# Performance work log

Hardware: AMD Instinct MI355X
Metric: run time of the kernel (lower is better)

The kernel has to match this reference:

```python
import jax, jax.numpy as jnp
import numpy as np

N, E, F_IN, H, C = 50000, 800000, 256, 64, 40
NEG_SLOPE = 0.2


def setup_inputs() -> dict:
    key = jax.random.key(0)
    ks = jax.random.split(key, 16)
    sc = lambda fan: 1.0 / np.sqrt(fan)
    return {
        "x": jax.random.normal(ks[0], (N, F_IN), dtype=jnp.float32),
        "edge_index": jax.random.randint(ks[1], (2, E), 0, N, dtype=jnp.int64),
        "W1l": jax.random.normal(ks[2], (F_IN, H), dtype=jnp.float32) * sc(F_IN),
        "b1l": jnp.zeros((H,), jnp.float32),
        "W1r": jax.random.normal(ks[3], (F_IN, H), dtype=jnp.float32) * sc(F_IN),
        "b1r": jnp.zeros((H,), jnp.float32),
        "att1": jax.random.normal(ks[4], (H,), dtype=jnp.float32) * sc(H),
        "bias1": jnp.zeros((H,), jnp.float32),
        "lin1_W": jax.random.normal(ks[5], (F_IN, H), dtype=jnp.float32) * sc(F_IN),
        "lin1_b": jnp.zeros((H,), jnp.float32),
        "W2l": jax.random.normal(ks[6], (H, C), dtype=jnp.float32) * sc(H),
        "b2l": jnp.zeros((C,), jnp.float32),
        "W2r": jax.random.normal(ks[7], (H, C), dtype=jnp.float32) * sc(H),
        "b2r": jnp.zeros((C,), jnp.float32),
        "att2": jax.random.normal(ks[8], (C,), dtype=jnp.float32) * sc(C),
        "bias2": jnp.zeros((C,), jnp.float32),
        "lin2_W": jax.random.normal(ks[9], (H, C), dtype=jnp.float32) * sc(H),
        "lin2_b": jnp.zeros((C,), jnp.float32),
    }


def gatv2_layer(x, src, dst, Wl, bl, Wr, br, att, bias, n):
    # PyG GATv2Conv, heads=1: xl = lin_l(x) (source), xr = lin_r(x) (target)
    xl = x @ Wl + bl                               # [n, out]
    xr = x @ Wr + br                               # [n, out]
    m = xl[src] + xr[dst]                          # [E, out] per-edge gather
    e = jax.nn.leaky_relu(m, NEG_SLOPE) @ att      # [E] attention logits
    # segment softmax over destination nodes (self-loops guarantee nonempty segments)
    emax = jax.ops.segment_max(e, dst, num_segments=n)
    ee = jnp.exp(e - emax[dst])
    denom = jax.ops.segment_sum(ee, dst, num_segments=n)
    alpha = ee / denom[dst]                        # [E]
    out = jax.ops.segment_sum(alpha[:, None] * xl[src], dst, num_segments=n)
    return out + bias


def reference(x, edge_index, W1l, b1l, W1r, b1r, att1, bias1, lin1_W, lin1_b,
              W2l, b2l, W2r, b2r, att2, bias2, lin2_W, lin2_b):
    n = x.shape[0]
    loops = jnp.arange(n, dtype=edge_index.dtype)
    src = jnp.concatenate([edge_index[0], loops])  # add_self_loops=True (PyG default)
    dst = jnp.concatenate([edge_index[1], loops])
    h = jax.nn.relu(gatv2_layer(x, src, dst, W1l, b1l, W1r, b1r, att1, bias1, n)
                    + x @ lin1_W + lin1_b)
    o = (gatv2_layer(h, src, dst, W2l, b2l, W2r, b2r, att2, bias2, n)
         + h @ lin2_W + lin2_b)
    return jax.nn.log_softmax(o, axis=1), edge_index
```

## Files before the change

kernel.cpp:

```cpp
#include <hip/hip_runtime.h>
#include <cmath>

#define NN 50000
#define NP 50048
#define NE 800000
#define CD 40
#define NEG_SLOPE 0.2f
#define NITEMS (NE + NN)
#define CHUNK 2048
#define NCH 416
#define NBKT 391
#define BCAP 3072
#define GB1 782
#define TB1 (3 * 64 * 256)
#define TB2 (3 * 64 * 64)
#define WPB 240

typedef __attribute__((ext_vector_type(8))) short s16x8;
typedef __attribute__((ext_vector_type(4))) float f32x4;
typedef __attribute__((ext_vector_type(2))) float f32x2;

__device__ __forceinline__ f32x2 pk_fma(f32x2 a, f32x2 b, f32x2 c) {
#if __has_builtin(__builtin_elementwise_fma)
  return __builtin_elementwise_fma(a, b, c);
#else
  f32x2 r; r[0] = fmaf(a[0], b[0], c[0]); r[1] = fmaf(a[1], b[1], c[1]); return r;
#endif
}
__device__ __forceinline__ f32x2 pk_max(f32x2 a, f32x2 b) {
#if __has_builtin(__builtin_elementwise_max)
  return __builtin_elementwise_max(a, b);
#else
  f32x2 r; r[0] = fmaxf(a[0], b[0]); r[1] = fmaxf(a[1], b[1]); return r;
#endif
}

__device__ __forceinline__ short f2bf(float x) {
  unsigned u = __builtin_bit_cast(unsigned, x);
  u += 0x7fffu + ((u >> 16) & 1u);
  return (short)(u >> 16);
}
__device__ __forceinline__ unsigned pack2(float lo, float hi) {
  return (unsigned)(unsigned short)f2bf(lo) | ((unsigned)(unsigned short)f2bf(hi) << 16);
}
__device__ __forceinline__ float bf2f_lo(unsigned v) {
  return __builtin_bit_cast(float, v << 16);
}
__device__ __forceinline__ float bf2f_hi(unsigned v) {
  return __builtin_bit_cast(float, v & 0xffff0000u);
}
__device__ __forceinline__ void ldbf8v(const unsigned short* p, f32x2* f) {
  const uint4 v = *reinterpret_cast<const uint4*>(p);
  f[0] = (f32x2){bf2f_lo(v.x), bf2f_hi(v.x)};
  f[1] = (f32x2){bf2f_lo(v.y), bf2f_hi(v.y)};
  f[2] = (f32x2){bf2f_lo(v.z), bf2f_hi(v.z)};
  f[3] = (f32x2){bf2f_lo(v.w), bf2f_hi(v.w)};
}

__global__ __launch_bounds__(256) void prep_bin(const float* __restrict__ W1l,
                                                const float* __restrict__ W1r,
                                                const float* __restrict__ L1,
                                                const float* __restrict__ W2l,
                                                const float* __restrict__ W2r,
                                                const float* __restrict__ L2,
                                                short* __restrict__ Wp1,
                                                short* __restrict__ Wp2,
                                                const int* __restrict__ ei,
                                                float* __restrict__ outE,
                                                int* __restrict__ gcur,
                                                unsigned* __restrict__ rec) {
  const int tid = threadIdx.x;
  if (blockIdx.x < WPB) {
    int e = blockIdx.x * 256 + tid;
    if (e < TB1) {
      int kb = e / 6144, r = e % 6144;
      int w = r / 2048, r2 = r % 2048;
      int t = r2 / 512, r3 = r2 % 512;
      int lane = r3 / 8, j = r3 % 8;
      int n = t * 16 + (lane & 15);
      int k = kb * 32 + (lane >> 4) * 8 + j;
      const float* W = (w == 0) ? W1l : (w == 1) ? W1r : L1;
      Wp1[e] = f2bf(W[k * 64 + n]);
    } else {
      e -= TB1;
      int kb = e / 6144, r = e % 6144;
      int w = r / 2048, r2 = r % 2048;
      int t = r2 / 512, r3 = r2 % 512;
      int lane = r3 / 8, j = r3 % 8;
      int n = t * 16 + (lane & 15);
      int k = kb * 32 + (lane >> 4) * 8 + j;
      const float* W = (w == 0) ? W2l : (w == 1) ? W2r : L2;
      Wp2[e] = (n < 40) ? f2bf(W[k * 40 + n]) : (short)0;
    }
    return;
  }
  __shared__ unsigned sorted[CHUNK];
  __shared__ int hist[512];
  __shared__ int bcur[512];
  __shared__ int gbase[512];
  const int base = (blockIdx.x - WPB) * CHUNK;
  for (int t = tid; t < 512; t += 256) { hist[t] = 0; bcur[t] = 0; gbase[t] = 0; }
  __syncthreads();
  unsigned key[CHUNK / 256];
#pragma unroll
  for (int u = 0; u < CHUNK / 256; ++u) {
    const int j = base + u * 256 + tid;
    unsigned k = 0xFFFFFFFFu;
    if (j < NITEMS) {
      int s, d;
      if (j < NE) {
        s = ei[j]; d = ei[NE + j];
        outE[j] = (float)s; outE[NE + j] = (float)d;
      } else {
        s = j - NE; d = s;
      }
      k = ((unsigned)d << 16) | (unsigned)s;
      atomicAdd(&hist[k >> 23], 1);
    }
    key[u] = k;
  }
  __syncthreads();
  if (tid < 64) {
    int carry = 0;
#pragma unroll
    for (int c = 0; c < 8; ++c) {
      int v = hist[c * 64 + tid];
      int inc = v;
#pragma unroll
      for (int off = 1; off < 64; off <<= 1) {
        int tt = __shfl_up(inc, off, 64);
        if (tid >= off) inc += tt;
      }
      hist[c * 64 + tid] = carry + inc - v;
      carry += __shfl(inc, 63, 64);
    }
  }
  __syncthreads();
#pragma unroll
  for (int u = 0; u < CHUNK / 256; ++u) {
    const unsigned k = key[u];
    if (k != 0xFFFFFFFFu) {
      const int b = k >> 23;
      sorted[hist[b] + atomicAdd(&bcur[b], 1)] = k;
    }
  }
  __syncthreads();
  for (int t = tid; t < NBKT; t += 256) {
    const int c = bcur[t];
    if (c > 0) gbase[t] = atomicAdd(&gcur[t], c);
  }
  __syncthreads();
  const int cnt = min(CHUNK, NITEMS - base);
  for (int i = tid; i < cnt; i += 256) {
    const unsigned k = sorted[i];
    const int b = k >> 23;
    const int p = gbase[b] + (i - hist[b]);
    if (p < BCAP) rec[(size_t)b * BCAP + p] = k;
  }
}

__device__ __forceinline__ void gemm1_body(int bid, const float* __restrict__ X,
                                           const short* __restrict__ Wp,
                                           const float* __restrict__ B0,
                                           const float* __restrict__ B1,
                                           const float* __restrict__ B2,
                                           unsigned short* __restrict__ Y0,
                                           unsigned short* __restrict__ Y1,
                                           unsigned short* __restrict__ Y2) {
  const int lane = threadIdx.x & 63;
  const int wave = threadIdx.x >> 6;
  const int r0 = bid * 64 + wave * 16;
  const int m = lane & 15;
  const int q = lane >> 4;
  f32x4 acc[3][4] = {};
  const float* a0 = X + (size_t)min(r0 + m, NN - 1) * 256 + q * 8;
  const short* bp = Wp + lane * 8;
#pragma unroll
  for (int kb = 0; kb < 8; ++kb) {
    const float4 v0 = *reinterpret_cast<const float4*>(a0 + kb * 32);
    const float4 v1 = *reinterpret_cast<const float4*>(a0 + kb * 32 + 4);
    s16x8 af0;
    af0[0] = f2bf(v0.x); af0[1] = f2bf(v0.y); af0[2] = f2bf(v0.z); af0[3] = f2bf(v0.w);
    af0[4] = f2bf(v1.x); af0[5] = f2bf(v1.y); af0[6] = f2bf(v1.z); af0[7] = f2bf(v1.w);
#pragma unroll
    for (int w = 0; w < 3; ++w) {
#pragma unroll
      for (int t = 0; t < 4; ++t) {
        const s16x8 bf = *reinterpret_cast<const s16x8*>(
            bp + (size_t)((kb * 3 + w) * 4 + t) * 512);
        acc[w][t] = __builtin_amdgcn_mfma_f32_16x16x32_bf16(af0, bf, acc[w][t], 0, 0, 0);
      }
    }
  }
#pragma unroll
  for (int w = 0; w < 3; ++w) {
    const float* B = (w == 0) ? B0 : (w == 1) ? B1 : B2;
    unsigned short* Y = (w == 0) ? Y0 : (w == 1) ? Y1 : Y2;
#pragma unroll
    for (int t = 0; t < 4; ++t) {
      const int c = t * 16 + m;
      const float bv = B[c];
#pragma unroll
      for (int rg = 0; rg < 4; ++rg) {
        const int row = r0 + q * 4 + rg;
        if (row < NN)
          Y[(size_t)row * 64 + c] = (unsigned short)f2bf(acc[w][t][rg] + bv);
      }
    }
  }
}

__global__ __launch_bounds__(256, 2) void build_gemm1(
    const float* __restrict__ X, const short* __restrict__ Wp1,
    const float* __restrict__ B0, const float* __restrict__ B1,
    const float* __restrict__ B2, unsigned short* __restrict__ Y0,
    unsigned short* __restrict__ Y1, unsigned short* __restrict__ Y2,
    const int* __restrict__ gcur, const unsigned* __restrict__ rec,
    int* __restrict__ offsets, unsigned short* __restrict__ csr16) {
  if (blockIdx.x < GB1) {
    gemm1_body(blockIdx.x, X, Wp1, B0, B1, B2, Y0, Y1, Y2);
    return;
  }
  const int b = blockIdx.x - GB1;
  const int tid = threadIdx.x;
  __shared__ unsigned recs[BCAP];
  __shared__ int red[256];
  __shared__ int cnt[128];
  __shared__ int sc[128];
  __shared__ int cur[128];
  int acc = 0;
  for (int t = tid; t < NBKT; t += 256)
    if (t < b) acc += gcur[t];
  red[tid] = acc;
  __syncthreads();
#pragma unroll
  for (int off = 128; off >= 1; off >>= 1) {
    if (tid < off) red[tid] += red[tid + off];
    __syncthreads();
  }
  const int base = red[0];
  const int Tb = min(gcur[b], BCAP);
  if (tid < 128) cnt[tid] = 0;
  __syncthreads();
  for (int i = tid; i < Tb; i += 256) {
    const unsigned k = rec[(size_t)b * BCAP + i];
    recs[i] = k;
    atomicAdd(&cnt[(k >> 16) & 127], 1);
  }
  __syncthreads();
  if (tid < 128) sc[tid] = cnt[tid];
  __syncthreads();
#pragma unroll
  for (int off = 1; off < 128; off <<= 1) {
    int v = (tid < 128 && tid >= off) ? sc[tid - off] : 0;
    __syncthreads();
    if (tid < 128) sc[tid] += v;
    __syncthreads();
  }
  if (tid < 128) {
    const int n = b * 128 + tid;
    if (n < NN) offsets[n + 1] = base + sc[tid];
    cur[tid] = sc[tid] - cnt[tid];
  }
  if (b == 0 && tid == 0) offsets[0] = 0;
  __syncthreads();
  for (int i = tid; i < Tb; i += 256) {
    const unsigned k = recs[i];
    const int p = atomicAdd(&cur[(k >> 16) & 127], 1);
    csr16[base + p] = (unsigned short)(k & 0xFFFFu);
  }
}

__global__ __launch_bounds__(256) void gemm2(const short* __restrict__ Xb,
                                             const short* __restrict__ Wp,
                                             const float* __restrict__ B0,
                                             const float* __restrict__ B1,
                                             const float* __restrict__ B2,
                                             unsigned short* __restrict__ Y0,
                                             unsigned short* __restrict__ Y1,
                                             unsigned short* __restrict__ Y2) {
  const int lane = threadIdx.x & 63;
  const int wave = threadIdx.x >> 6;
  const int r0 = blockIdx.x * 64 + wave * 16;
  const int m = lane & 15;
  const int q = lane >> 4;
  f32x4 acc[3][4] = {};
  const short* a0 = Xb + (size_t)(r0 + m) * 64 + q * 8;
  const short* bp = Wp + lane * 8;
#pragma unroll
  for (int kb = 0; kb < 2; ++kb) {
    const s16x8 af0 = *reinterpret_cast<const s16x8*>(a0 + kb * 32);
#pragma unroll
    for (int w = 0; w < 3; ++w) {
#pragma unroll
      for (int t = 0; t < 4; ++t) {
        const s16x8 bf = *reinterpret_cast<const s16x8*>(
            bp + (size_t)((kb * 3 + w) * 4 + t) * 512);
        acc[w][t] = __builtin_amdgcn_mfma_f32_16x16x32_bf16(af0, bf, acc[w][t], 0, 0, 0);
      }
    }
  }
#pragma unroll
  for (int w = 0; w < 3; ++w) {
    const float* B = (w == 0) ? B0 : (w == 1) ? B1 : B2;
    unsigned short* Y = (w == 0) ? Y0 : (w == 1) ? Y1 : Y2;
#pragma unroll
    for (int t = 0; t < 4; ++t) {
      const int c = t * 16 + m;
      const float bv = (c < 40) ? B[c] : 0.f;
#pragma unroll
      for (int rg = 0; rg < 4; ++rg) {
        const int row = r0 + q * 4 + rg;
        if (row < NN)
          Y[(size_t)row * 64 + c] = (unsigned short)f2bf(acc[w][t][rg] + bv);
      }
    }
  }
}

template <int OC, bool FINAL>
__global__ __launch_bounds__(256) void gat_agg(const unsigned short* __restrict__ XL,
                                               const unsigned short* __restrict__ XR,
                                               const unsigned short* __restrict__ XLIN,
                                               const float* __restrict__ att,
                                               const float* __restrict__ bias,
                                               const int* __restrict__ offsets,
                                               const unsigned short* __restrict__ csr,
                                               float* __restrict__ out,
                                               unsigned short* __restrict__ outb) {
  const int lane = threadIdx.x & 63;
  const int g = lane >> 3;
  const int l = lane & 7;
  const int d = blockIdx.x * 4 + (threadIdx.x >> 6);
  if (d >= NN) return;
  const bool dimok = (8 * l < OC);
  f32x2 a2[4] = {};
  if (dimok) {
    const float4 t0 = *reinterpret_cast<const float4*>(&att[8 * l]);
    const float4 t1 = *reinterpret_cast<const float4*>(&att[8 * l + 4]);
    a2[0] = (f32x2){t0.x, t0.y}; a2[1] = (f32x2){t0.z, t0.w};
    a2[2] = (f32x2){t1.x, t1.y}; a2[3] = (f32x2){t1.z, t1.w};
  }
  f32x2 xr2[4];
  ldbf8v(XR + (size_t)d * 64 + 8 * l, xr2);
  const int beg = offsets[d];
  const int end = offsets[d + 1];
  float D = 0.f;
  f32x2 A2[4] = {};
  const f32x2 ns = (f32x2){NEG_SLOPE, NEG_SLOPE};
  const int nit = (end - beg + 7) >> 3;
  const int i0 = beg + g;
  int sa = (int)csr[(i0 < end) ? i0 : beg];
  for (int it = 0; it < nit; ++it) {
    const int icur = beg + it * 8 + g;
    const bool act = (icur < end);
    f32x2 xl2[4];
    ldbf8v(XL + (size_t)sa * 64 + 8 * l, xl2);
    const int inext = icur + 8;
    sa = (int)csr[(inext < end) ? inext : beg];
    f32x2 pacc = (f32x2){0.f, 0.f};
#pragma unroll
    for (int j = 0; j < 4; ++j) {
      const f32x2 t = xl2[j] + xr2[j];
      const f32x2 lr = pk_max(t, t * ns);
      pacc = pk_fma(lr, a2[j], pacc);
    }
    float p = pacc[0] + pacc[1];
    p += __shfl_xor(p, 1, 64);
    p += __shfl_xor(p, 2, 64);
    p += __shfl_xor(p, 4, 64);
    const float w = __expf(act ? p : -INFINITY);
    D += w;
    const f32x2 w2 = (f32x2){w, w};
#pragma unroll
    for (int j = 0; j < 4; ++j) A2[j] = pk_fma(w2, xl2[j], A2[j]);
  }
  D += __shfl_xor(D, 8, 64);
  D += __shfl_xor(D, 16, 64);
  D += __shfl_xor(D, 32, 64);
  float A[8];
#pragma unroll
  for (int j = 0; j < 4; ++j) {
#pragma unroll
    for (int c = 0; c < 2; ++c) {
      float v = A2[j][c];
      v += __shfl_xor(v, 8, 64);
      v += __shfl_xor(v, 16, 64);
      v += __shfl_xor(v, 32, 64);
      A[j * 2 + c] = v;
    }
  }
  f32x2 xlin2[4];
  ldbf8v(XLIN + (size_t)d * 64 + 8 * l, xlin2);
  float b[8] = {};
  if (dimok) {
    const float4 t0 = *reinterpret_cast<const float4*>(&bias[8 * l]);
    const float4 t1 = *reinterpret_cast<const float4*>(&bias[8 * l + 4]);
    b[0] = t0.x; b[1] = t0.y; b[2] = t0.z; b[3] = t0.w;
    b[4] = t1.x; b[5] = t1.y; b[6] = t1.z; b[7] = t1.w;
  }
  const float inv = 1.0f / D;
  float val[8];
#pragma unroll
  for (int j = 0; j < 8; ++j)
    val[j] = fmaf(A[j], inv, b[j]) + xlin2[j >> 1][j & 1];
  if (!FINAL) {
    if (g == 0) {
      uint4 o;
      o.x = pack2(fmaxf(val[0], 0.f), fmaxf(val[1], 0.f));
      o.y = pack2(fmaxf(val[2], 0.f), fmaxf(val[3], 0.f));
      o.z = pack2(fmaxf(val[4], 0.f), fmaxf(val[5], 0.f));
      o.w = pack2(fmaxf(val[6], 0.f), fmaxf(val[7], 0.f));
      *reinterpret_cast<uint4*>(&outb[(size_t)d * 64 + 8 * l]) = o;
    }
  } else {
    float mx = -3e38f;
    if (dimok) {
#pragma unroll
      for (int j = 0; j < 8; ++j) mx = fmaxf(mx, val[j]);
    }
    mx = fmaxf(mx, __shfl_xor(mx, 1, 64));
    mx = fmaxf(mx, __shfl_xor(mx, 2, 64));
    mx = fmaxf(mx, __shfl_xor(mx, 4, 64));
    float es = 0.f;
    if (dimok) {
#pragma unroll
      for (int j = 0; j < 8; ++j) es += __expf(val[j] - mx);
    }
    es += __shfl_xor(es, 1, 64);
    es += __shfl_xor(es, 2, 64);
    es += __shfl_xor(es, 4, 64);
    const float lse = mx + __logf(es);
    if (g == 0 && dimok) {
      float4 o0, o1;
      o0.x = val[0] - lse; o0.y = val[1] - lse; o0.z = val[2] - lse; o0.w = val[3] - lse;
      o1.x = val[4] - lse; o1.y = val[5] - lse; o1.z = val[6] - lse; o1.w = val[7] - lse;
      float* dst = &out[(size_t)d * OC + 8 * l];
      *reinterpret_cast<float4*>(dst) = o0;
      *reinterpret_cast<float4*>(dst + 4) = o1;
    }
  }
}

extern "C" void kernel_launch(void* const* d_in, const int* in_sizes, int n_in,
                              void* d_out, int out_size, void* d_ws, size_t ws_size,
                              hipStream_t stream) {
  const float* x     = (const float*)d_in[0];
  const int*   ei    = (const int*)d_in[1];
  const float* W1l   = (const float*)d_in[2];
  const float* b1l   = (const float*)d_in[3];
  const float* W1r   = (const float*)d_in[4];
  const float* b1r   = (const float*)d_in[5];
  const float* att1  = (const float*)d_in[6];
  const float* bias1 = (const float*)d_in[7];
  const float* lin1W = (const float*)d_in[8];
  const float* lin1b = (const float*)d_in[9];
  const float* W2l   = (const float*)d_in[10];
  const float* b2l   = (const float*)d_in[11];
  const float* W2r   = (const float*)d_in[12];
  const float* b2r   = (const float*)d_in[13];
  const float* att2  = (const float*)d_in[14];
  const float* bias2 = (const float*)d_in[15];
  const float* lin2W = (const float*)d_in[16];
  const float* lin2b = (const float*)d_in[17];
  float* out = (float*)d_out;

  char* ws = (char*)d_ws;
  size_t off = 0;
  auto alloc = [&](size_t bytes) -> void* {
    void* p = ws + off;
    off += (bytes + 255) & ~(size_t)255;
    return p;
  };
  short* Wp1 = (short*)alloc((size_t)TB1 * 2);
  short* Wp2 = (short*)alloc((size_t)TB2 * 2);
  unsigned short* XL1   = (unsigned short*)alloc((size_t)NN * 64 * 2);
  unsigned short* XR1   = (unsigned short*)alloc((size_t)NN * 64 * 2);
  unsigned short* XLIN1 = (unsigned short*)alloc((size_t)NN * 64 * 2);
  unsigned short* Hb    = (unsigned short*)alloc((size_t)NP * 64 * 2);
  unsigned short* XL2   = (unsigned short*)alloc((size_t)NN * 64 * 2);
  unsigned short* XR2   = (unsigned short*)alloc((size_t)NN * 64 * 2);
  unsigned short* XLIN2 = (unsigned short*)alloc((size_t)NN * 64 * 2);
  int* gcur    = (int*)alloc((size_t)NBKT * 4);
  int* offsets = (int*)alloc((size_t)(NN + 1) * 4);
  unsigned* rec = (unsigned*)alloc((size_t)NBKT * BCAP * 4);
  unsigned short* csr = (unsigned short*)alloc((size_t)NITEMS * 2);

  hipMemsetAsync(gcur, 0, (size_t)NBKT * 4, stream);
  prep_bin<<<WPB + NCH, 256, 0, stream>>>(W1l, W1r, lin1W, W2l, W2r, lin2W,
                                          Wp1, Wp2, ei, out + (size_t)NN * CD,
                                          gcur, rec);
  build_gemm1<<<GB1 + NBKT, 256, 0, stream>>>(x, Wp1, b1l, b1r, lin1b,
                                              XL1, XR1, XLIN1, gcur, rec,
                                              offsets, csr);
  gat_agg<64, false><<<(NN + 3) / 4, 256, 0, stream>>>(XL1, XR1, XLIN1, att1,
                                                       bias1, offsets, csr,
                                                       nullptr, Hb);
  gemm2<<<GB1, 256, 0, stream>>>((const short*)Hb, Wp2, b2l, b2r, lin2b,
                                 XL2, XR2, XLIN2);
  gat_agg<40, true><<<(NN + 3) / 4, 256, 0, stream>>>(XL2, XR2, XLIN2, att2,
                                                      bias2, offsets, csr,
                                                      out, nullptr);
}
```

Baseline: 243.8 us.

## Software-pipeline loads in GEMM and edge-aggregation kernels

New measurement: 234.4 us. 1.04x faster.

```diff
diff --git a/kernel.cpp b/kernel.cpp
--- a/kernel.cpp
+++ b/kernel.cpp
@@ -49,8 +49,7 @@
 __device__ __forceinline__ float bf2f_hi(unsigned v) {
   return __builtin_bit_cast(float, v & 0xffff0000u);
 }
-__device__ __forceinline__ void ldbf8v(const unsigned short* p, f32x2* f) {
-  const uint4 v = *reinterpret_cast<const uint4*>(p);
+__device__ __forceinline__ void unp8(uint4 v, f32x2* f) {
   f[0] = (f32x2){bf2f_lo(v.x), bf2f_hi(v.x)};
   f[1] = (f32x2){bf2f_lo(v.y), bf2f_hi(v.y)};
   f[2] = (f32x2){bf2f_lo(v.z), bf2f_hi(v.z)};
@@ -175,22 +174,25 @@
   f32x4 acc[3][4] = {};
   const float* a0 = X + (size_t)min(r0 + m, NN - 1) * 256 + q * 8;
   const short* bp = Wp + lane * 8;
+  float4 v0 = *reinterpret_cast<const float4*>(a0);
+  float4 v1 = *reinterpret_cast<const float4*>(a0 + 4);
 #pragma unroll
   for (int kb = 0; kb < 8; ++kb) {
-    const float4 v0 = *reinterpret_cast<const float4*>(a0 + kb * 32);
-    const float4 v1 = *reinterpret_cast<const float4*>(a0 + kb * 32 + 4);
-    s16x8 af0;
-    af0[0] = f2bf(v0.x); af0[1] = f2bf(v0.y); af0[2] = f2bf(v0.z); af0[3] = f2bf(v0.w);
-    af0[4] = f2bf(v1.x); af0[5] = f2bf(v1.y); af0[6] = f2bf(v1.z); af0[7] = f2bf(v1.w);
-#pragma unroll
-    for (int w = 0; w < 3; ++w) {
-#pragma unroll
-      for (int t = 0; t < 4; ++t) {
-        const s16x8 bf = *reinterpret_cast<const s16x8*>(
-            bp + (size_t)((kb * 3 + w) * 4 + t) * 512);
-        acc[w][t] = __builtin_amdgcn_mfma_f32_16x16x32_bf16(af0, bf, acc[w][t], 0, 0, 0);
-      }
-    }
+    s16x8 bf[12];
+#pragma unroll
+    for (int i = 0; i < 12; ++i)
+      bf[i] = *reinterpret_cast<const s16x8*>(bp + (size_t)(kb * 12 + i) * 512);
+    s16x8 af;
+    af[0] = f2bf(v0.x); af[1] = f2bf(v0.y); af[2] = f2bf(v0.z); af[3] = f2bf(v0.w);
+    af[4] = f2bf(v1.x); af[5] = f2bf(v1.y); af[6] = f2bf(v1.z); af[7] = f2bf(v1.w);
+    if (kb < 7) {
+      v0 = *reinterpret_cast<const float4*>(a0 + (kb + 1) * 32);
+      v1 = *reinterpret_cast<const float4*>(a0 + (kb + 1) * 32 + 4);
+    }
+#pragma unroll
+    for (int i = 0; i < 12; ++i)
+      acc[i >> 2][i & 3] = __builtin_amdgcn_mfma_f32_16x16x32_bf16(
+          af, bf[i], acc[i >> 2][i & 3], 0, 0, 0);
   }
 #pragma unroll
   for (int w = 0; w < 3; ++w) {
@@ -271,14 +273,14 @@
   }
 }
 
-__global__ __launch_bounds__(256) void gemm2(const short* __restrict__ Xb,
-                                             const short* __restrict__ Wp,
-                                             const float* __restrict__ B0,
-                                             const float* __restrict__ B1,
-                                             const float* __restrict__ B2,
-                                             unsigned short* __restrict__ Y0,
-                                             unsigned short* __restrict__ Y1,
-                                             unsigned short* __restrict__ Y2) {
+__global__ __launch_bounds__(256, 2) void gemm2(const short* __restrict__ Xb,
+                                                const short* __restrict__ Wp,
+                                                const float* __restrict__ B0,
+                                                const float* __restrict__ B1,
+                                                const float* __restrict__ B2,
+                                                unsigned short* __restrict__ Y0,
+                                                unsigned short* __restrict__ Y1,
+                                                unsigned short* __restrict__ Y2) {
   const int lane = threadIdx.x & 63;
   const int wave = threadIdx.x >> 6;
   const int r0 = blockIdx.x * 64 + wave * 16;
@@ -289,16 +291,15 @@
   const short* bp = Wp + lane * 8;
 #pragma unroll
   for (int kb = 0; kb < 2; ++kb) {
-    const s16x8 af0 = *reinterpret_cast<const s16x8*>(a0 + kb * 32);
-#pragma unroll
-    for (int w = 0; w < 3; ++w) {
-#pragma unroll
-      for (int t = 0; t < 4; ++t) {
-        const s16x8 bf = *reinterpret_cast<const s16x8*>(
-            bp + (size_t)((kb * 3 + w) * 4 + t) * 512);
-        acc[w][t] = __builtin_amdgcn_mfma_f32_16x16x32_bf16(af0, bf, acc[w][t], 0, 0, 0);
-      }
-    }
+    s16x8 bf[12];
+#pragma unroll
+    for (int i = 0; i < 12; ++i)
+      bf[i] = *reinterpret_cast<const s16x8*>(bp + (size_t)(kb * 12 + i) * 512);
+    const s16x8 af = *reinterpret_cast<const s16x8*>(a0 + kb * 32);
+#pragma unroll
+    for (int i = 0; i < 12; ++i)
+      acc[i >> 2][i & 3] = __builtin_amdgcn_mfma_f32_16x16x32_bf16(
+          af, bf[i], acc[i >> 2][i & 3], 0, 0, 0);
   }
 #pragma unroll
   for (int w = 0; w < 3; ++w) {
@@ -342,7 +343,7 @@
     a2[2] = (f32x2){t1.x, t1.y}; a2[3] = (f32x2){t1.z, t1.w};
   }
   f32x2 xr2[4];
-  ldbf8v(XR + (size_t)d * 64 + 8 * l, xr2);
+  unp8(*reinterpret_cast<const uint4*>(XR + (size_t)d * 64 + 8 * l), xr2);
   const int beg = offsets[d];
   const int end = offsets[d + 1];
   float D = 0.f;
@@ -351,13 +352,17 @@
   const int nit = (end - beg + 7) >> 3;
   const int i0 = beg + g;
   int sa = (int)csr[(i0 < end) ? i0 : beg];
+  uint4 raw_next = *reinterpret_cast<const uint4*>(XL + (size_t)sa * 64 + 8 * l);
+  const int i1 = i0 + 8;
+  sa = (int)csr[(i1 < end) ? i1 : beg];
   for (int it = 0; it < nit; ++it) {
-    const int icur = beg + it * 8 + g;
-    const bool act = (icur < end);
+    const uint4 raw = raw_next;
+    const bool act = (beg + it * 8 + g) < end;
+    raw_next = *reinterpret_cast<const uint4*>(XL + (size_t)sa * 64 + 8 * l);
+    const int i2 = beg + (it + 2) * 8 + g;
+    sa = (int)csr[(i2 < end) ? i2 : beg];
     f32x2 xl2[4];
-    ldbf8v(XL + (size_t)sa * 64 + 8 * l, xl2);
-    const int inext = icur + 8;
-    sa = (int)csr[(inext < end) ? inext : beg];
+    unp8(raw, xl2);
     f32x2 pacc = (f32x2){0.f, 0.f};
 #pragma unroll
     for (int j = 0; j < 4; ++j) {
@@ -391,7 +396,7 @@
     }
   }
   f32x2 xlin2[4];
-  ldbf8v(XLIN + (size_t)d * 64 + 8 * l, xlin2);
+  unp8(*reinterpret_cast<const uint4*>(XLIN + (size_t)d * 64 + 8 * l), xlin2);
   float b[8] = {};
   if (dimok) {
     const float4 t0 = *reinterpret_cast<const float4*>(&bias[8 * l]);
```
